# Kernel tuning notes

Hardware: AMD Instinct MI355X
Metric: run time of the kernel (lower is better)

The kernel has to match this reference:

```python
import jax, jax.numpy as jnp
import numpy as np

N = 50000
E = 625000
D_IN = 128
D_OUT = 128
NEG_SLOPE = 0.01  # torch LeakyReLU default


def setup_inputs() -> dict:
    key = jax.random.key(0)
    k1, k2, k3, k4, k5, k6, k7, k8 = jax.random.split(key, 8)
    features = jax.random.normal(k1, (N, D_IN), dtype=jnp.float32)
    target = jax.random.randint(k2, (E,), 0, N, dtype=jnp.int64)
    neighbor = jax.random.randint(k3, (E,), 0, N, dtype=jnp.int64)
    values = jax.random.uniform(k4, (E,), dtype=jnp.float32)
    # nn.Linear params (kaiming-uniform-ish init: U(-1/sqrt(in), 1/sqrt(in)))
    bound = 1.0 / np.sqrt(D_IN)
    W1 = jax.random.uniform(k5, (D_OUT, D_IN), minval=-bound, maxval=bound, dtype=jnp.float32)
    b1 = jax.random.uniform(k6, (D_OUT,), minval=-bound, maxval=bound, dtype=jnp.float32)
    W2 = jax.random.uniform(k7, (D_OUT, D_IN), minval=-bound, maxval=bound, dtype=jnp.float32)
    b2 = jax.random.uniform(k8, (D_OUT,), minval=-bound, maxval=bound, dtype=jnp.float32)
    return {"features": features, "target": target, "neighbor": neighbor,
            "values": values, "W1": W1, "b1": b1, "W2": W2, "b2": b2}


def reference(features, target, neighbor, values, W1, b1, W2, b2):
    # gather-scale: msg[e] = features[neighbor[e]] * values[e]
    msg = features[neighbor] * values[:, None]              # (E, D_IN)
    # scatter-add into target nodes
    h_neigh = jax.ops.segment_sum(msg, target, num_segments=N)  # (N, D_IN)
    # dual linear fusion + leaky relu
    h = (features + h_neigh) @ W1.T + b1 + (features * h_neigh) @ W2.T + b2
    return jnp.where(h >= 0, h, NEG_SLOPE * h)
```

## Files before the change

### kernel.cpp

```cpp
#include <hip/hip_runtime.h>

#define D 128
#define CAP 40
#define NEG_SLOPE 0.01f

typedef float v4f __attribute__((ext_vector_type(4)));
typedef short short8 __attribute__((ext_vector_type(8)));

static __device__ __forceinline__ short f2bf(float f) {
    unsigned u = __float_as_uint(f);
    unsigned r = (u + 0x7fffu + ((u >> 16) & 1u)) >> 16;
    return (short)r;
}
static __device__ __forceinline__ float bflo(unsigned u) { return __uint_as_float(u << 16); }
static __device__ __forceinline__ float bfhi(unsigned u) { return __uint_as_float(u & 0xffff0000u); }
static __device__ __forceinline__ unsigned packbf(float x, float y) {
    return (unsigned)(unsigned short)f2bf(x) | ((unsigned)(unsigned short)f2bf(y) << 16);
}

__global__ __launch_bounds__(256) void convbucket_kernel(const float* __restrict__ feat,
                                                         const float* __restrict__ W1,
                                                         const float* __restrict__ W2,
                                                         const int* __restrict__ tgt,
                                                         const int* __restrict__ nbr,
                                                         const float* __restrict__ vals,
                                                         unsigned* __restrict__ featbf,
                                                         short* __restrict__ Wbf,
                                                         int* __restrict__ deg,
                                                         int2* __restrict__ edata,
                                                         int nPairs, int E) {
    int i = blockIdx.x * 256 + threadIdx.x;
    if (i < nPairs) {
        float2 f = ((const float2*)feat)[i];
        featbf[i] = packbf(f.x, f.y);
    }
    if (i < D * D) {
        Wbf[i]         = f2bf(W1[i]);
        Wbf[D * D + i] = f2bf(W2[i]);
    }
    if (i < E) {
        int t    = tgt[i];
        int slot = atomicAdd(&deg[t], 1);
        if (slot < CAP) {
            int2 ed;
            ed.x = nbr[i];
            ed.y = __float_as_int(vals[i]);
            edata[(long)t * CAP + slot] = ed;
        }
    }
}

__global__ __launch_bounds__(256) void gather_kernel(const unsigned* __restrict__ featbf,
                                                     const int2* __restrict__ edata,
                                                     const int* __restrict__ deg,
                                                     const int* __restrict__ tgt,
                                                     const int* __restrict__ nbr,
                                                     const float* __restrict__ vals,
                                                     unsigned* __restrict__ X1,
                                                     unsigned* __restrict__ X2,
                                                     int nNodes, int E) {
    int wid  = (blockIdx.x * 256 + threadIdx.x) >> 6;
    int lane = threadIdx.x & 63;
    if (wid >= nNodes) return;
    int d = deg[wid];

    unsigned uf = featbf[(long)wid * (D / 2) + lane];

    float ax0 = 0.f, ay0 = 0.f, ax1 = 0.f, ay1 = 0.f;
    float ax2 = 0.f, ay2 = 0.f, ax3 = 0.f, ay3 = 0.f;

    if (d <= CAP) {
        const int2* ep = edata + (long)wid * CAP;
        int dm1 = d - 1;
        for (int j = 0; j < d; j += 8) {
            int2 p0 = ep[min(j + 0, dm1)];
            int2 p1 = ep[min(j + 1, dm1)];
            int2 p2 = ep[min(j + 2, dm1)];
            int2 p3 = ep[min(j + 3, dm1)];
            int2 p4 = ep[min(j + 4, dm1)];
            int2 p5 = ep[min(j + 5, dm1)];
            int2 p6 = ep[min(j + 6, dm1)];
            int2 p7 = ep[min(j + 7, dm1)];
            unsigned u0 = featbf[(long)p0.x * (D / 2) + lane];
            unsigned u1 = featbf[(long)p1.x * (D / 2) + lane];
            unsigned u2 = featbf[(long)p2.x * (D / 2) + lane];
            unsigned u3 = featbf[(long)p3.x * (D / 2) + lane];
            unsigned u4 = featbf[(long)p4.x * (D / 2) + lane];
            unsigned u5 = featbf[(long)p5.x * (D / 2) + lane];
            unsigned u6 = featbf[(long)p6.x * (D / 2) + lane];
            unsigned u7 = featbf[(long)p7.x * (D / 2) + lane];
            float v0 = (j + 0 < d) ? __int_as_float(p0.y) : 0.0f;
            float v1 = (j + 1 < d) ? __int_as_float(p1.y) : 0.0f;
            float v2 = (j + 2 < d) ? __int_as_float(p2.y) : 0.0f;
            float v3 = (j + 3 < d) ? __int_as_float(p3.y) : 0.0f;
            float v4 = (j + 4 < d) ? __int_as_float(p4.y) : 0.0f;
            float v5 = (j + 5 < d) ? __int_as_float(p5.y) : 0.0f;
            float v6 = (j + 6 < d) ? __int_as_float(p6.y) : 0.0f;
            float v7 = (j + 7 < d) ? __int_as_float(p7.y) : 0.0f;
            ax0 += bflo(u0) * v0; ay0 += bfhi(u0) * v0;
            ax1 += bflo(u1) * v1; ay1 += bfhi(u1) * v1;
            ax2 += bflo(u2) * v2; ay2 += bfhi(u2) * v2;
            ax3 += bflo(u3) * v3; ay3 += bfhi(u3) * v3;
            ax0 += bflo(u4) * v4; ay0 += bfhi(u4) * v4;
            ax1 += bflo(u5) * v5; ay1 += bfhi(u5) * v5;
            ax2 += bflo(u6) * v6; ay2 += bfhi(u6) * v6;
            ax3 += bflo(u7) * v7; ay3 += bfhi(u7) * v7;
        }
    } else {
        for (int base = 0; base < E; base += 64) {
            int e = base + lane;
            int t = (e < E) ? tgt[e] : -1;
            unsigned long long m = __ballot(t == wid);
            while (m) {
                int b = __ffsll((long long)m) - 1;
                m &= m - 1;
                int   ee = base + b;
                int   nb = nbr[ee];
                float v  = vals[ee];
                unsigned u = featbf[(long)nb * (D / 2) + lane];
                ax0 += bflo(u) * v;
                ay0 += bfhi(u) * v;
            }
        }
    }

    float accx = (ax0 + ax1) + (ax2 + ax3);
    float accy = (ay0 + ay1) + (ay2 + ay3);
    float fx = bflo(uf), fy = bfhi(uf);
    X1[(long)wid * (D / 2) + lane] = packbf(fx + accx, fy + accy);
    X2[(long)wid * (D / 2) + lane] = packbf(fx * accx, fy * accy);
}

__global__ __launch_bounds__(512) void gemm_kernel(const short* __restrict__ X1s,
                                                   const short* __restrict__ X2s,
                                                   const short* __restrict__ Wbf,
                                                   const float* __restrict__ b1,
                                                   const float* __restrict__ b2,
                                                   float* __restrict__ out, int nNodes) {
    __shared__ __align__(16) short sW[2 * D * D];

    int tid = threadIdx.x;
    for (int c = tid; c < 4096; c += 512) {
        int r  = c >> 4;
        int cc = c & 15;
        int pp = cc ^ (r & 15);
        *(short8*)(&sW[r * D + pp * 8]) = *(const short8*)(Wbf + c * 8);
    }
    __syncthreads();

    int lane = tid & 63;
    int wid  = (blockIdx.x * 512 + tid) >> 6;
    int m0   = wid * 32;
    if (m0 >= nNodes) return;
    bool t2 = (m0 + 16) < nNodes;

    int mrow = lane & 15;
    int quad = lane >> 4;

    float bias[8];
#pragma unroll
    for (int ot = 0; ot < 8; ot++) {
        int o = ot * 16 + mrow;
        bias[ot] = b1[o] + b2[o];
    }

    const short* xa1 = X1s + (long)(m0 + mrow) * D + quad * 8;
    const short* xa2 = X2s + (long)(m0 + mrow) * D + quad * 8;
    const short* xb1 = xa1 + 16 * D;
    const short* xb2 = xa2 + 16 * D;

    v4f acc[2][8];
#pragma unroll
    for (int t = 0; t < 2; t++)
#pragma unroll
        for (int i = 0; i < 8; i++) acc[t][i] = (v4f)(0.0f);

#pragma unroll
    for (int s = 0; s < 4; s++) {
        short8 a1 = *(const short8*)(xa1 + s * 32);
        short8 a2 = *(const short8*)(xa2 + s * 32);
        short8 c1, c2;
        if (t2) {
            c1 = *(const short8*)(xb1 + s * 32);
            c2 = *(const short8*)(xb2 + s * 32);
        }
        int pp = (s * 4 + quad) ^ mrow;
#pragma unroll
        for (int ot = 0; ot < 8; ot++) {
            int row = ot * 16 + mrow;
            short8 w1 = *(const short8*)(&sW[row * D + pp * 8]);
            short8 w2 = *(const short8*)(&sW[D * D + row * D + pp * 8]);
            acc[0][ot] = __builtin_amdgcn_mfma_f32_16x16x32_bf16(a1, w1, acc[0][ot], 0, 0, 0);
            acc[0][ot] = __builtin_amdgcn_mfma_f32_16x16x32_bf16(a2, w2, acc[0][ot], 0, 0, 0);
            if (t2) {
                acc[1][ot] = __builtin_amdgcn_mfma_f32_16x16x32_bf16(c1, w1, acc[1][ot], 0, 0, 0);
                acc[1][ot] = __builtin_amdgcn_mfma_f32_16x16x32_bf16(c2, w2, acc[1][ot], 0, 0, 0);
            }
        }
    }

#pragma unroll
    for (int ot = 0; ot < 8; ot++) {
        int o = ot * 16 + mrow;
#pragma unroll
        for (int r = 0; r < 4; r++) {
            int   node = m0 + quad * 4 + r;
            float v    = acc[0][ot][r] + bias[ot];
            out[(long)node * D + o] = (v >= 0.0f) ? v : NEG_SLOPE * v;
            if (t2) {
                float w = acc[1][ot][r] + bias[ot];
                out[(long)(node + 16) * D + o] = (w >= 0.0f) ? w : NEG_SLOPE * w;
            }
        }
    }
}

extern "C" void kernel_launch(void* const* d_in, const int* in_sizes, int n_in,
                              void* d_out, int out_size, void* d_ws, size_t ws_size,
                              hipStream_t stream) {
    const float* feat = (const float*)d_in[0];
    const int*   tgt  = (const int*)d_in[1];
    const int*   nbr  = (const int*)d_in[2];
    const float* vals = (const float*)d_in[3];
    const float* W1   = (const float*)d_in[4];
    const float* b1   = (const float*)d_in[5];
    const float* W2   = (const float*)d_in[6];
    const float* b2   = (const float*)d_in[7];
    float*       out  = (float*)d_out;

    int E      = in_sizes[1];
    int nNodes = out_size / D;

    int*      deg    = (int*)d_ws;
    int2*     edata  = (int2*)(deg + nNodes);
    short*    Wbf    = (short*)(edata + (long)nNodes * CAP);
    unsigned* featbf = (unsigned*)(Wbf + 2 * D * D);
    unsigned* X1     = featbf + (long)nNodes * (D / 2);
    unsigned* X2     = X1 + (long)nNodes * (D / 2);

    int nPairs = nNodes * (D / 2);

    hipMemsetAsync(deg, 0, (size_t)nNodes * sizeof(int), stream);
    convbucket_kernel<<<(nPairs + 255) / 256, 256, 0, stream>>>(feat, W1, W2, tgt, nbr, vals,
                                                                featbf, Wbf, deg, edata, nPairs, E);
    gather_kernel<<<(nNodes * 64 + 255) / 256, 256, 0, stream>>>(featbf, edata, deg, tgt, nbr, vals,
                                                                 X1, X2, nNodes, E);

    int nPairTiles = (nNodes + 31) / 32;
    int nBlocks    = (nPairTiles + 7) / 8;
    gemm_kernel<<<nBlocks, 512, 0, stream>>>((const short*)X1, (const short*)X2, Wbf, b1, b2, out, nNodes);
}
```

Before: 171.9 us.

## Shrink per-node edge buckets and add compact overflow list for high-degree nodes

```diff
diff --git a/kernel.cpp b/kernel.cpp
--- a/kernel.cpp
+++ b/kernel.cpp
@@ -1,7 +1,8 @@
 #include <hip/hip_runtime.h>
 
 #define D 128
-#define CAP 40
+#define CAP 24
+#define EPT 8
 #define NEG_SLOPE 0.01f
 
 typedef float v4f __attribute__((ext_vector_type(4)));
@@ -28,24 +29,42 @@
                                                          short* __restrict__ Wbf,
                                                          int* __restrict__ deg,
                                                          int2* __restrict__ edata,
-                                                         int nPairs, int E) {
-    int i = blockIdx.x * 256 + threadIdx.x;
-    if (i < nPairs) {
-        float2 f = ((const float2*)feat)[i];
-        featbf[i] = packbf(f.x, f.y);
-    }
-    if (i < D * D) {
-        Wbf[i]         = f2bf(W1[i]);
-        Wbf[D * D + i] = f2bf(W2[i]);
-    }
-    if (i < E) {
-        int t    = tgt[i];
-        int slot = atomicAdd(&deg[t], 1);
-        if (slot < CAP) {
-            int2 ed;
-            ed.x = nbr[i];
-            ed.y = __float_as_int(vals[i]);
-            edata[(long)t * CAP + slot] = ed;
+                                                         int4* __restrict__ ovf,
+                                                         int* __restrict__ ovf_cnt,
+                                                         int nPairs, int E, int nbB) {
+    if ((int)blockIdx.x < nbB) {
+        int base = (blockIdx.x * 256 + threadIdx.x) * EPT;
+#pragma unroll
+        for (int k = 0; k < EPT; k++) {
+            int e = base + k;
+            if (e < E) {
+                int t    = tgt[e];
+                int slot = atomicAdd(&deg[t], 1);
+                if (slot < CAP) {
+                    int2 ed;
+                    ed.x = nbr[e];
+                    ed.y = __float_as_int(vals[e]);
+                    edata[(long)t * CAP + slot] = ed;
+                } else {
+                    int o = atomicAdd(ovf_cnt, 1);
+                    int4 ov;
+                    ov.x = t;
+                    ov.y = nbr[e];
+                    ov.z = __float_as_int(vals[e]);
+                    ov.w = 0;
+                    ovf[o] = ov;
+                }
+            }
+        }
+    } else {
+        int i = (blockIdx.x - nbB) * 256 + threadIdx.x;
+        if (i < nPairs) {
+            float2 f = ((const float2*)feat)[i];
+            featbf[i] = packbf(f.x, f.y);
+        }
+        if (i < D * D) {
+            Wbf[i]         = f2bf(W1[i]);
+            Wbf[D * D + i] = f2bf(W2[i]);
         }
     }
 }
@@ -53,26 +72,26 @@
 __global__ __launch_bounds__(256) void gather_kernel(const unsigned* __restrict__ featbf,
                                                      const int2* __restrict__ edata,
                                                      const int* __restrict__ deg,
-                                                     const int* __restrict__ tgt,
-                                                     const int* __restrict__ nbr,
-                                                     const float* __restrict__ vals,
+                                                     const int4* __restrict__ ovf,
+                                                     const int* __restrict__ ovf_cnt,
                                                      unsigned* __restrict__ X1,
                                                      unsigned* __restrict__ X2,
-                                                     int nNodes, int E) {
+                                                     int nNodes) {
     int wid  = (blockIdx.x * 256 + threadIdx.x) >> 6;
     int lane = threadIdx.x & 63;
     if (wid >= nNodes) return;
-    int d = deg[wid];
+    int d  = deg[wid];
+    int dd = d < CAP ? d : CAP;
 
     unsigned uf = featbf[(long)wid * (D / 2) + lane];
 
     float ax0 = 0.f, ay0 = 0.f, ax1 = 0.f, ay1 = 0.f;
     float ax2 = 0.f, ay2 = 0.f, ax3 = 0.f, ay3 = 0.f;
 
-    if (d <= CAP) {
+    {
         const int2* ep = edata + (long)wid * CAP;
-        int dm1 = d - 1;
-        for (int j = 0; j < d; j += 8) {
+        int dm1 = dd - 1;
+        for (int j = 0; j < dd; j += 8) {
             int2 p0 = ep[min(j + 0, dm1)];
             int2 p1 = ep[min(j + 1, dm1)];
             int2 p2 = ep[min(j + 2, dm1)];
@@ -89,14 +108,14 @@
             unsigned u5 = featbf[(long)p5.x * (D / 2) + lane];
             unsigned u6 = featbf[(long)p6.x * (D / 2) + lane];
             unsigned u7 = featbf[(long)p7.x * (D / 2) + lane];
-            float v0 = (j + 0 < d) ? __int_as_float(p0.y) : 0.0f;
-            float v1 = (j + 1 < d) ? __int_as_float(p1.y) : 0.0f;
-            float v2 = (j + 2 < d) ? __int_as_float(p2.y) : 0.0f;
-            float v3 = (j + 3 < d) ? __int_as_float(p3.y) : 0.0f;
-            float v4 = (j + 4 < d) ? __int_as_float(p4.y) : 0.0f;
-            float v5 = (j + 5 < d) ? __int_as_float(p5.y) : 0.0f;
-            float v6 = (j + 6 < d) ? __int_as_float(p6.y) : 0.0f;
-            float v7 = (j + 7 < d) ? __int_as_float(p7.y) : 0.0f;
+            float v0 = (j + 0 < dd) ? __int_as_float(p0.y) : 0.0f;
+            float v1 = (j + 1 < dd) ? __int_as_float(p1.y) : 0.0f;
+            float v2 = (j + 2 < dd) ? __int_as_float(p2.y) : 0.0f;
+            float v3 = (j + 3 < dd) ? __int_as_float(p3.y) : 0.0f;
+            float v4 = (j + 4 < dd) ? __int_as_float(p4.y) : 0.0f;
+            float v5 = (j + 5 < dd) ? __int_as_float(p5.y) : 0.0f;
+            float v6 = (j + 6 < dd) ? __int_as_float(p6.y) : 0.0f;
+            float v7 = (j + 7 < dd) ? __int_as_float(p7.y) : 0.0f;
             ax0 += bflo(u0) * v0; ay0 += bfhi(u0) * v0;
             ax1 += bflo(u1) * v1; ay1 += bfhi(u1) * v1;
             ax2 += bflo(u2) * v2; ay2 += bfhi(u2) * v2;
@@ -106,18 +125,20 @@
             ax2 += bflo(u6) * v6; ay2 += bfhi(u6) * v6;
             ax3 += bflo(u7) * v7; ay3 += bfhi(u7) * v7;
         }
-    } else {
-        for (int base = 0; base < E; base += 64) {
-            int e = base + lane;
-            int t = (e < E) ? tgt[e] : -1;
+    }
+
+    if (d > CAP) {
+        int cnt = *ovf_cnt;
+        for (int basek = 0; basek < cnt; basek += 64) {
+            int k = basek + lane;
+            int t = (k < cnt) ? ovf[k].x : -1;
             unsigned long long m = __ballot(t == wid);
             while (m) {
                 int b = __ffsll((long long)m) - 1;
                 m &= m - 1;
-                int   ee = base + b;
-                int   nb = nbr[ee];
-                float v  = vals[ee];
-                unsigned u = featbf[(long)nb * (D / 2) + lane];
+                int4  ov = ovf[basek + b];
+                float v  = __int_as_float(ov.z);
+                unsigned u = featbf[(long)ov.y * (D / 2) + lane];
                 ax0 += bflo(u) * v;
                 ay0 += bfhi(u) * v;
             }
@@ -231,20 +252,25 @@
     int E      = in_sizes[1];
     int nNodes = out_size / D;
 
-    int*      deg    = (int*)d_ws;
-    int2*     edata  = (int2*)(deg + nNodes);
-    short*    Wbf    = (short*)(edata + (long)nNodes * CAP);
-    unsigned* featbf = (unsigned*)(Wbf + 2 * D * D);
-    unsigned* X1     = featbf + (long)nNodes * (D / 2);
-    unsigned* X2     = X1 + (long)nNodes * (D / 2);
+    int*      deg     = (int*)d_ws;
+    int*      ovf_cnt = deg + nNodes;
+    int4*     ovf     = (int4*)(deg + nNodes + 4);
+    int2*     edata   = (int2*)(ovf + E);
+    short*    Wbf     = (short*)(edata + (long)nNodes * CAP);
+    unsigned* featbf  = (unsigned*)(Wbf + 2 * D * D);
+    unsigned* X1      = featbf + (long)nNodes * (D / 2);
+    unsigned* X2      = X1 + (long)nNodes * (D / 2);
 
     int nPairs = nNodes * (D / 2);
-
-    hipMemsetAsync(deg, 0, (size_t)nNodes * sizeof(int), stream);
-    convbucket_kernel<<<(nPairs + 255) / 256, 256, 0, stream>>>(feat, W1, W2, tgt, nbr, vals,
-                                                                featbf, Wbf, deg, edata, nPairs, E);
-    gather_kernel<<<(nNodes * 64 + 255) / 256, 256, 0, stream>>>(featbf, edata, deg, tgt, nbr, vals,
-                                                                 X1, X2, nNodes, E);
+    int nbB    = (E + 256 * EPT - 1) / (256 * EPT);
+    int nbC    = (nPairs + 255) / 256;
+
+    hipMemsetAsync(deg, 0, (size_t)(nNodes + 4) * sizeof(int), stream);
+    convbucket_kernel<<<nbB + nbC, 256, 0, stream>>>(feat, W1, W2, tgt, nbr, vals,
+                                                     featbf, Wbf, deg, edata, ovf, ovf_cnt,
+                                                     nPairs, E, nbB);
+    gather_kernel<<<(nNodes * 64 + 255) / 256, 256, 0, stream>>>(featbf, edata, deg, ovf, ovf_cnt,
+                                                                 X1, X2, nNodes);
 
     int nPairTiles = (nNodes + 31) / 32;
     int nBlocks    = (nPairTiles + 7) / 8;
```

After: 169.9 us. About the same (-1.2%).
